# Optimization experiments

Measured on AMD Instinct MI355X. Metric: run time of the kernel, lower is better.

The kernel has to match this reference:

```python
import jax, jax.numpy as jnp
import numpy as np
from jax import lax

B, CIN, COUT, WDIM, K, H, W_ = 8, 512, 512, 512, 3, 64, 64

def setup_inputs() -> dict:
    key = jax.random.key(0)
    ks = jax.random.split(key, 7)
    x = jax.random.normal(ks[0], (B, CIN, H, W_), dtype=jnp.float32)
    w = jax.random.normal(ks[1], (B, WDIM), dtype=jnp.float32)
    noise = jax.random.normal(ks[2], (B, COUT, H, W_), dtype=jnp.float32)
    # params (kaiming-ish scale for weight; demodulation normalizes anyway)
    weight = jax.random.normal(ks[3], (1, COUT, CIN, K, K), dtype=jnp.float32) * 0.05
    affine_w = jax.random.normal(ks[4], (CIN, WDIM), dtype=jnp.float32) * (1.0 / np.sqrt(WDIM))
    affine_b = jnp.zeros((CIN,), dtype=jnp.float32)
    bias = jnp.zeros((COUT,), dtype=jnp.float32)
    return {"x": x, "w": w, "noise": noise, "weight": weight,
            "affine_w": affine_w, "affine_b": affine_b, "bias": bias}

def reference(x, w, noise, weight, affine_w, affine_b, bias):
    b, cin, h, ww = x.shape
    cout, k = weight.shape[1], weight.shape[3]
    # style: affine(w) + 1
    s = jnp.einsum('bd,cd->bc', w, affine_w) + affine_b          # [B, Cin]
    s = s[:, None, :, None, None] + 1.0                           # [B,1,Cin,1,1]
    w_mod = weight * s                                            # [B,Cout,Cin,k,k]
    d = lax.rsqrt(jnp.sum(w_mod * w_mod, axis=(2, 3, 4), keepdims=True) + 1e-8)
    w_mod = w_mod * d
    # grouped conv: groups = B
    x_ = x.reshape(1, b * cin, h, ww)
    w_ = w_mod.reshape(b * cout, cin, k, k)
    pad = k // 2
    y = lax.conv_general_dilated(
        x_, w_, window_strides=(1, 1), padding=[(pad, pad), (pad, pad)],
        feature_group_count=b,
        dimension_numbers=('NCHW', 'OIHW', 'NCHW'))
    y = y.reshape(b, cout, h, ww)
    y = y + noise + bias[None, :, None, None]
    return jnp.where(y >= 0, y, 0.2 * y)
```

## Files before the change

### kernel.cpp

```cpp
#include <hip/hip_runtime.h>
#include <hip/hip_bf16.h>


#define CIN   512
#define COUT  512
#define KDIM  4608
#define HWPIX 4096

typedef __attribute__((ext_vector_type(8))) __bf16 bf16x8;
typedef __attribute__((ext_vector_type(4))) float  f32x4;

__device__ __forceinline__ unsigned short f2bf(float f){
  union { float f; unsigned int u; } v; v.f = f;
  unsigned int u = v.u;
  u += 0x7fffu + ((u >> 16) & 1u);
  return (unsigned short)(u >> 16);
}

#define GLDS16(g, l) __builtin_amdgcn_global_load_lds(                      \
    (const __attribute__((address_space(1))) unsigned int*)(g),             \
    (__attribute__((address_space(3))) unsigned int*)(l), 16, 0, 0)

__global__ void style_k(const float* __restrict__ w, const float* __restrict__ aw,
                        const float* __restrict__ ab, float* __restrict__ styles){
  int wid = threadIdx.x >> 6, lane = threadIdx.x & 63;
  int gid = blockIdx.x * 4 + wid;
  int b = gid >> 9, c = gid & 511;
  const float* wb = w + b * 512;
  const float* ar = aw + c * 512;
  float sum = 0.f;
  for (int j = lane; j < 512; j += 64) sum += wb[j] * ar[j];
  for (int off = 32; off; off >>= 1) sum += __shfl_down(sum, off, 64);
  if (lane == 0) styles[gid] = sum + ab[c] + 1.0f;
}

__global__ void modw_k(const float* __restrict__ weight, const float* __restrict__ styles,
                       unsigned short* __restrict__ wmod){
  int o = blockIdx.x;
  int b = blockIdx.y;
  int t = threadIdx.x;
  const float* wrow = weight + (size_t)o * KDIM;
  const float* st = styles + b * 512;
  __shared__ unsigned short sw[9 * 520];
  __shared__ float red[4];
  int wid = t >> 6, lane = t & 63;
  float vals[18];
  float part = 0.f;
#pragma unroll
  for (int it = 0; it < 9; ++it){
    int e = (it * 256 + t) * 2;
    float2 v2 = *(const float2*)(wrow + e);
    int i0 = e / 9, i1 = (e + 1) / 9;
    float a0 = v2.x * st[i0];
    float a1 = v2.y * st[i1];
    vals[2 * it] = a0; vals[2 * it + 1] = a1;
    part += a0 * a0 + a1 * a1;
  }
  for (int off = 32; off; off >>= 1) part += __shfl_down(part, off, 64);
  if (lane == 0) red[wid] = part;
  __syncthreads();
  float d = rsqrtf(red[0] + red[1] + red[2] + red[3] + 1e-8f);
#pragma unroll
  for (int it = 0; it < 9; ++it){
    int e = (it * 256 + t) * 2;
    int i0 = e / 9, i1 = (e + 1) / 9;
    int tap0 = e - i0 * 9, tap1 = e + 1 - i1 * 9;
    sw[tap0 * 520 + i0] = f2bf(vals[2 * it] * d);
    sw[tap1 * 520 + i1] = f2bf(vals[2 * it + 1] * d);
  }
  __syncthreads();
  unsigned int* orow32 = (unsigned int*)(wmod + ((size_t)(b * 512 + o)) * KDIM);
#pragma unroll
  for (int it = 0; it < 9; ++it){
    int u = it * 256 + t;
    int e = u * 2;
    int tap2 = e >> 9, i2 = e & 511;
    orow32[u] = *(const unsigned int*)&sw[tap2 * 520 + i2];
  }
}

__global__ void xpose_k(const float* __restrict__ x, unsigned short* __restrict__ xpad){
  int h = blockIdx.x, cg = blockIdx.y, b = blockIdx.z;
  int c0 = cg * 64;
  __shared__ unsigned short lds[64][66];
  int t = threadIdx.x;
  const float* xb = x + (((size_t)(b * 512 + c0)) * 64 + h) * 64;
#pragma unroll
  for (int it = 0; it < 4; ++it){
    int idx = it * 256 + t;
    int cl = idx >> 4, w4 = (idx & 15) * 4;
    float4 v = *(const float4*)(xb + (size_t)cl * 4096 + w4);
    lds[w4 + 0][cl] = f2bf(v.x);
    lds[w4 + 1][cl] = f2bf(v.y);
    lds[w4 + 2][cl] = f2bf(v.z);
    lds[w4 + 3][cl] = f2bf(v.w);
  }
  if (t < 64){
    int which = t >> 5;
    int ch2 = (t & 31) * 2;
    int wl = which ? 65 : 0;
    *(unsigned int*)&xpad[(((size_t)b * 66 + h + 1) * 66 + wl) * 512 + c0 + ch2] = 0u;
  }
  if (h == 0 || h == 63){
    int row = (h == 0) ? 0 : 65;
    for (int u = t; u < 66 * 32; u += 256){
      int wl = u >> 5, ch2 = (u & 31) * 2;
      *(unsigned int*)&xpad[(((size_t)b * 66 + row) * 66 + wl) * 512 + c0 + ch2] = 0u;
    }
  }
  __syncthreads();
#pragma unroll
  for (int it = 0; it < 2; ++it){
    int idx = it * 256 + t;
    int wl = idx >> 3, ch = idx & 7;
    unsigned int u0 = *(const unsigned int*)&lds[wl][ch * 8 + 0];
    unsigned int u1 = *(const unsigned int*)&lds[wl][ch * 8 + 2];
    unsigned int u2 = *(const unsigned int*)&lds[wl][ch * 8 + 4];
    unsigned int u3 = *(const unsigned int*)&lds[wl][ch * 8 + 6];
    int off = ((b * 66 + h + 1) * 66 + (wl + 1)) * 512 + c0 + ch * 8;
    *(uint4*)&xpad[off] = make_uint4(u0, u1, u2, u3);
  }
}

__device__ __forceinline__ int bshift_of(int t){
  int tap = t >> 3;
  int dy = (tap * 11) >> 5;
  int dx = tap - dy * 3;
  return (((dy - 1) * 66 + (dx - 1)) << 9) + ((t & 7) << 6);
}

__global__ __launch_bounds__(512, 2) void conv_gemm(
    const unsigned short* __restrict__ wmod, const unsigned short* __restrict__ xpad,
    const float* __restrict__ noise, const float* __restrict__ bias,
    float* __restrict__ out){
  __shared__ unsigned short As[4][128 * 64];
  __shared__ unsigned short Bs[4][128 * 64];
  int g = blockIdx.x;
  int b = g & 7, sl = g >> 3;
  int mt = sl >> 4, nt = sl & 15;
  int m0 = mt * 256, n0 = nt * 256, h0 = nt * 4;
  int tid = threadIdx.x, lane = tid & 63, wid = tid >> 6;
  int wmp = wid >> 2, wnp = wid & 3;
  int lf = lane & 15, lg = lane >> 4;

  const unsigned short* wbase = wmod + ((size_t)(b * 512 + m0)) * KDIM;
  const unsigned short* xb    = xpad + (size_t)b * (66 * 66 * 512);

  int srow  = tid >> 3;
  int sc    = (tid & 7) ^ (srow & 7);
  int aoffg  = srow * KDIM + sc * 8;
  int boffg0 = ((h0 + 1) * 66 + srow + 1) * 512 + sc * 8;
  int boffg1 = ((h0 + 2) * 66 + srow + 1) * 512 + sc * 8;

  int arow[4], brow[2];
#pragma unroll
  for (int i = 0; i < 4; ++i) arow[i] = (wmp * 64 + i * 16 + lf) * 64;
#pragma unroll
  for (int j = 0; j < 2; ++j) brow[j] = (wnp * 32 + j * 16 + lf) * 64;
  int pch0 = ((lg    ) ^ (lane & 7)) * 8;
  int pch1 = ((lg + 4) ^ (lane & 7)) * 8;

  f32x4 acc[2][2][4][2];
#pragma unroll
  for (int a0 = 0; a0 < 2; ++a0)
#pragma unroll
    for (int a1 = 0; a1 < 2; ++a1)
#pragma unroll
      for (int a2 = 0; a2 < 4; ++a2)
#pragma unroll
        for (int a3 = 0; a3 < 2; ++a3) acc[a0][a1][a2][a3] = (f32x4){0.f, 0.f, 0.f, 0.f};

  bf16x8 af[4][2], bq0[2][2], bq1[2][2];

#define SBAR0() __builtin_amdgcn_sched_barrier(0)

#define STAGE_A(t_, h_, s_) do {                                              \
    const unsigned short* gpa_ = wbase + (size_t)(h_) * (128 * KDIM) + (t_) * 64; \
    GLDS16(gpa_ + aoffg,             &As[s_][tid * 8]);                       \
    GLDS16(gpa_ + aoffg + 64 * KDIM, &As[s_][(512 + tid) * 8]);               \
  } while (0)

#define STAGE_B(t_, h_, s_) do {                                              \
    const unsigned short* gpb_ = xb + (h_) * (2 * 66 * 512) + bshift_of(t_);  \
    GLDS16(gpb_ + boffg0, &Bs[s_][tid * 8]);                                  \
    GLDS16(gpb_ + boffg1, &Bs[s_][(512 + tid) * 8]);                          \
  } while (0)

#define LOAD_A(s_) do {                                                       \
    _Pragma("unroll") for (int fi_ = 0; fi_ < 4; ++fi_){                      \
      af[fi_][0] = *(const bf16x8*)&As[s_][arow[fi_] + pch0];                 \
      af[fi_][1] = *(const bf16x8*)&As[s_][arow[fi_] + pch1]; }               \
  } while (0)

#define LOAD_B(s_, B_) do {                                                   \
    _Pragma("unroll") for (int fj_ = 0; fj_ < 2; ++fj_){                      \
      B_[fj_][0] = *(const bf16x8*)&Bs[s_][brow[fj_] + pch0];                 \
      B_[fj_][1] = *(const bf16x8*)&Bs[s_][brow[fj_] + pch1]; }               \
  } while (0)

#define MFMA_Q(MH_, NH_, B_) do {                                             \
    __builtin_amdgcn_s_setprio(1);                                            \
    _Pragma("unroll") for (int fi_ = 0; fi_ < 4; ++fi_)                       \
    _Pragma("unroll") for (int fj_ = 0; fj_ < 2; ++fj_){                      \
      acc[MH_][NH_][fi_][fj_] = __builtin_amdgcn_mfma_f32_16x16x32_bf16(      \
          af[fi_][0], B_[fj_][0], acc[MH_][NH_][fi_][fj_], 0, 0, 0);          \
      acc[MH_][NH_][fi_][fj_] = __builtin_amdgcn_mfma_f32_16x16x32_bf16(      \
          af[fi_][1], B_[fj_][1], acc[MH_][NH_][fi_][fj_], 0, 0, 0); }        \
    __builtin_amdgcn_s_setprio(0);                                            \
  } while (0)

#define SYNC_MID() do { SBAR0(); __builtin_amdgcn_s_barrier();                \
    asm volatile("s_waitcnt lgkmcnt(0)" ::: "memory"); SBAR0(); } while (0)
#define SYNC_END() do { SBAR0(); __builtin_amdgcn_s_barrier(); } while (0)
#define VMW6() asm volatile("s_waitcnt vmcnt(6)" ::: "memory")
#define VMW0() asm volatile("s_waitcnt vmcnt(0)" ::: "memory")

  STAGE_A(0, 0, 0); STAGE_B(0, 0, 0); STAGE_B(0, 1, 1); STAGE_A(0, 1, 1);
  STAGE_A(1, 0, 2); STAGE_B(1, 0, 2); STAGE_B(1, 1, 3);
  VMW6();
  __builtin_amdgcn_s_barrier();

#pragma unroll 1
  for (int it = 0; it < 35; ++it){
    int T = it * 2;
    LOAD_A(0); LOAD_B(0, bq0);
    STAGE_A(T + 1, 1, 3);
    SYNC_MID(); MFMA_Q(0, 0, bq0); SYNC_END();
    LOAD_B(1, bq1);
    STAGE_A(T + 2, 0, 0);
    SYNC_MID(); MFMA_Q(0, 1, bq1); SYNC_END();
    LOAD_A(1);
    STAGE_B(T + 2, 0, 0);
    SYNC_MID(); MFMA_Q(1, 0, bq0); SYNC_END();
    STAGE_B(T + 2, 1, 1);
    VMW6();
    SYNC_MID(); MFMA_Q(1, 1, bq1); SYNC_END();
    LOAD_A(2); LOAD_B(2, bq0);
    STAGE_A(T + 2, 1, 1);
    SYNC_MID(); MFMA_Q(0, 0, bq0); SYNC_END();
    LOAD_B(3, bq1);
    STAGE_A(T + 3, 0, 2);
    SYNC_MID(); MFMA_Q(0, 1, bq1); SYNC_END();
    LOAD_A(3);
    STAGE_B(T + 3, 0, 2);
    SYNC_MID(); MFMA_Q(1, 0, bq0); SYNC_END();
    STAGE_B(T + 3, 1, 3);
    VMW6();
    SYNC_MID(); MFMA_Q(1, 1, bq1); SYNC_END();
  }

  LOAD_A(0); LOAD_B(0, bq0);
  STAGE_A(71, 1, 3);
  SYNC_MID(); MFMA_Q(0, 0, bq0); SYNC_END();
  LOAD_B(1, bq1);
  SYNC_MID(); MFMA_Q(0, 1, bq1); SYNC_END();
  LOAD_A(1);
  SYNC_MID(); MFMA_Q(1, 0, bq0); SYNC_END();
  VMW0();
  SYNC_MID(); MFMA_Q(1, 1, bq1); SYNC_END();
  LOAD_A(2); LOAD_B(2, bq0);
  SYNC_MID(); MFMA_Q(0, 0, bq0); SYNC_END();
  LOAD_B(3, bq1);
  SYNC_MID(); MFMA_Q(0, 1, bq1); SYNC_END();
  LOAD_A(3);
  SYNC_MID(); MFMA_Q(1, 0, bq0); SYNC_END();
  SYNC_MID(); MFMA_Q(1, 1, bq1);

#undef STAGE_A
#undef STAGE_B
#undef LOAD_A
#undef LOAD_B
#undef MFMA_Q
#undef SYNC_MID
#undef SYNC_END
#undef VMW6
#undef VMW0
#undef SBAR0

#pragma unroll
  for (int MH = 0; MH < 2; ++MH)
#pragma unroll
    for (int NH = 0; NH < 2; ++NH)
#pragma unroll
      for (int fi = 0; fi < 4; ++fi)
#pragma unroll
        for (int fj = 0; fj < 2; ++fj){
          int o_base = m0 + MH * 128 + wmp * 64 + fi * 16 + lg * 4;
          int n = n0 + NH * 128 + wnp * 32 + fj * 16 + lf;
#pragma unroll
          for (int r = 0; r < 4; ++r){
            int o = o_base + r;
            size_t idx = ((size_t)(b * 512 + o)) * HWPIX + n;
            float v = acc[MH][NH][fi][fj][r] + noise[idx] + bias[o];
            out[idx] = (v >= 0.f) ? v : 0.2f * v;
          }
        }
}

extern "C" void kernel_launch(void* const* d_in, const int* in_sizes, int n_in,
                              void* d_out, int out_size, void* d_ws, size_t ws_size,
                              hipStream_t stream) {
  const float* x        = (const float*)d_in[0];
  const float* w        = (const float*)d_in[1];
  const float* noise    = (const float*)d_in[2];
  const float* weight   = (const float*)d_in[3];
  const float* affine_w = (const float*)d_in[4];
  const float* affine_b = (const float*)d_in[5];
  const float* bias     = (const float*)d_in[6];
  float* out = (float*)d_out;

  float* styles = (float*)d_ws;
  unsigned short* wmod = (unsigned short*)((char*)d_ws + 16384);
  unsigned short* xpad = (unsigned short*)((char*)d_ws + 16384 + 37748736ull);

  style_k<<<dim3(1024), 256, 0, stream>>>(w, affine_w, affine_b, styles);
  modw_k <<<dim3(512, 8), 256, 0, stream>>>(weight, styles, wmod);
  xpose_k<<<dim3(64, 8, 8), 256, 0, stream>>>(x, xpad);
  conv_gemm<<<dim3(256), 512, 0, stream>>>(wmod, xpad, noise, bias, out);
}
```

Before: 326.5 us.

## Double-buffer A fragments and overlap LDS reads with MFMA phases

Adds a second register buffer for A fragments so the LDS reads for the next phase are issued before the current MFMA block. Partial lgkmcnt waits replace full waits, and one of the two barriers per phase is dropped. The global-to-LDS staging order and vmcnt thresholds are rearranged to match. This aims to hide LDS latency and barrier stalls behind matrix work, at the cost of more VGPRs and tighter reliance on getting the wait counts right.

```diff
diff --git a/kernel.cpp b/kernel.cpp
--- a/kernel.cpp
+++ b/kernel.cpp
@@ -170,7 +170,7 @@
 #pragma unroll
         for (int a3 = 0; a3 < 2; ++a3) acc[a0][a1][a2][a3] = (f32x4){0.f, 0.f, 0.f, 0.f};
 
-  bf16x8 af[4][2], bq0[2][2], bq1[2][2];
+  bf16x8 af0[4][2], af1[4][2], bq0[2][2], bq1[2][2];
 
 #define SBAR0() __builtin_amdgcn_sched_barrier(0)
 
@@ -186,94 +186,97 @@
     GLDS16(gpb_ + boffg1, &Bs[s_][(512 + tid) * 8]);                          \
   } while (0)
 
-#define LOAD_A(s_) do {                                                       \
-    _Pragma("unroll") for (int fi_ = 0; fi_ < 4; ++fi_){                      \
-      af[fi_][0] = *(const bf16x8*)&As[s_][arow[fi_] + pch0];                 \
-      af[fi_][1] = *(const bf16x8*)&As[s_][arow[fi_] + pch1]; }               \
-  } while (0)
-
-#define LOAD_B(s_, B_) do {                                                   \
+#define LOAD_AF1(AF_, s_, fi_) do {                                           \
+    AF_[fi_][0] = *(const bf16x8*)&As[s_][arow[fi_] + pch0];                  \
+    AF_[fi_][1] = *(const bf16x8*)&As[s_][arow[fi_] + pch1];                  \
+  } while (0)
+
+#define LOAD_BQ(B_, s_) do {                                                  \
     _Pragma("unroll") for (int fj_ = 0; fj_ < 2; ++fj_){                      \
       B_[fj_][0] = *(const bf16x8*)&Bs[s_][brow[fj_] + pch0];                 \
       B_[fj_][1] = *(const bf16x8*)&Bs[s_][brow[fj_] + pch1]; }               \
   } while (0)
 
-#define MFMA_Q(MH_, NH_, B_) do {                                             \
+#define MFMA_Q(MH_, NH_, AF_, B_) do {                                        \
     __builtin_amdgcn_s_setprio(1);                                            \
     _Pragma("unroll") for (int fi_ = 0; fi_ < 4; ++fi_)                       \
     _Pragma("unroll") for (int fj_ = 0; fj_ < 2; ++fj_){                      \
       acc[MH_][NH_][fi_][fj_] = __builtin_amdgcn_mfma_f32_16x16x32_bf16(      \
-          af[fi_][0], B_[fj_][0], acc[MH_][NH_][fi_][fj_], 0, 0, 0);          \
+          AF_[fi_][0], B_[fj_][0], acc[MH_][NH_][fi_][fj_], 0, 0, 0);         \
       acc[MH_][NH_][fi_][fj_] = __builtin_amdgcn_mfma_f32_16x16x32_bf16(      \
-          af[fi_][1], B_[fj_][1], acc[MH_][NH_][fi_][fj_], 0, 0, 0); }        \
+          AF_[fi_][1], B_[fj_][1], acc[MH_][NH_][fi_][fj_], 0, 0, 0); }       \
     __builtin_amdgcn_s_setprio(0);                                            \
   } while (0)
 
-#define SYNC_MID() do { SBAR0(); __builtin_amdgcn_s_barrier();                \
+#define TAIL6() do { SBAR0();                                                 \
+    asm volatile("s_waitcnt lgkmcnt(6)" ::: "memory"); SBAR0(); } while (0)
+#define TAIL0() do { SBAR0();                                                 \
     asm volatile("s_waitcnt lgkmcnt(0)" ::: "memory"); SBAR0(); } while (0)
-#define SYNC_END() do { SBAR0(); __builtin_amdgcn_s_barrier(); } while (0)
-#define VMW6() asm volatile("s_waitcnt vmcnt(6)" ::: "memory")
+#define PH_END() do { SBAR0(); __builtin_amdgcn_s_barrier(); } while (0)
+#define VMW4() asm volatile("s_waitcnt vmcnt(4)" ::: "memory")
 #define VMW0() asm volatile("s_waitcnt vmcnt(0)" ::: "memory")
 
-  STAGE_A(0, 0, 0); STAGE_B(0, 0, 0); STAGE_B(0, 1, 1); STAGE_A(0, 1, 1);
-  STAGE_A(1, 0, 2); STAGE_B(1, 0, 2); STAGE_B(1, 1, 3);
-  VMW6();
+  STAGE_A(0, 0, 0); STAGE_A(0, 1, 1); STAGE_B(0, 0, 0); STAGE_B(0, 1, 1);
+  STAGE_A(1, 0, 2); STAGE_B(1, 0, 2); STAGE_B(1, 1, 3); STAGE_A(1, 1, 3);
+  VMW0();
   __builtin_amdgcn_s_barrier();
+  LOAD_AF1(af0, 0, 0); LOAD_AF1(af0, 0, 1); LOAD_AF1(af0, 0, 2); LOAD_AF1(af0, 0, 3);
+  LOAD_BQ(bq0, 0);
 
 #pragma unroll 1
   for (int it = 0; it < 35; ++it){
     int T = it * 2;
-    LOAD_A(0); LOAD_B(0, bq0);
-    STAGE_A(T + 1, 1, 3);
-    SYNC_MID(); MFMA_Q(0, 0, bq0); SYNC_END();
-    LOAD_B(1, bq1);
-    STAGE_A(T + 2, 0, 0);
-    SYNC_MID(); MFMA_Q(0, 1, bq1); SYNC_END();
-    LOAD_A(1);
-    STAGE_B(T + 2, 0, 0);
-    SYNC_MID(); MFMA_Q(1, 0, bq0); SYNC_END();
+    LOAD_BQ(bq1, 1); LOAD_AF1(af1, 1, 0);
+    TAIL6(); MFMA_Q(0, 0, af0, bq0); PH_END();
+    STAGE_A(T + 2, 0, 0); STAGE_B(T + 2, 0, 0);
+    LOAD_AF1(af1, 1, 1); LOAD_AF1(af1, 1, 2); LOAD_AF1(af1, 1, 3);
+    TAIL6(); MFMA_Q(0, 1, af0, bq1); PH_END();
     STAGE_B(T + 2, 1, 1);
-    VMW6();
-    SYNC_MID(); MFMA_Q(1, 1, bq1); SYNC_END();
-    LOAD_A(2); LOAD_B(2, bq0);
+    LOAD_AF1(af0, 2, 0); LOAD_AF1(af0, 2, 1); LOAD_AF1(af0, 2, 2);
+    TAIL6(); MFMA_Q(1, 0, af1, bq0); PH_END();
     STAGE_A(T + 2, 1, 1);
-    SYNC_MID(); MFMA_Q(0, 0, bq0); SYNC_END();
-    LOAD_B(3, bq1);
-    STAGE_A(T + 3, 0, 2);
-    SYNC_MID(); MFMA_Q(0, 1, bq1); SYNC_END();
-    LOAD_A(3);
-    STAGE_B(T + 3, 0, 2);
-    SYNC_MID(); MFMA_Q(1, 0, bq0); SYNC_END();
+    VMW4();
+    LOAD_BQ(bq0, 2); LOAD_AF1(af0, 2, 3);
+    TAIL6(); MFMA_Q(1, 1, af1, bq1); PH_END();
+    LOAD_BQ(bq1, 3); LOAD_AF1(af1, 3, 0);
+    TAIL6(); MFMA_Q(0, 0, af0, bq0); PH_END();
+    STAGE_A(T + 3, 0, 2); STAGE_B(T + 3, 0, 2);
+    LOAD_AF1(af1, 3, 1); LOAD_AF1(af1, 3, 2); LOAD_AF1(af1, 3, 3);
+    TAIL6(); MFMA_Q(0, 1, af0, bq1); PH_END();
     STAGE_B(T + 3, 1, 3);
-    VMW6();
-    SYNC_MID(); MFMA_Q(1, 1, bq1); SYNC_END();
-  }
-
-  LOAD_A(0); LOAD_B(0, bq0);
-  STAGE_A(71, 1, 3);
-  SYNC_MID(); MFMA_Q(0, 0, bq0); SYNC_END();
-  LOAD_B(1, bq1);
-  SYNC_MID(); MFMA_Q(0, 1, bq1); SYNC_END();
-  LOAD_A(1);
-  SYNC_MID(); MFMA_Q(1, 0, bq0); SYNC_END();
+    LOAD_AF1(af0, 0, 0); LOAD_AF1(af0, 0, 1); LOAD_AF1(af0, 0, 2);
+    TAIL6(); MFMA_Q(1, 0, af1, bq0); PH_END();
+    STAGE_A(T + 3, 1, 3);
+    VMW4();
+    LOAD_BQ(bq0, 0); LOAD_AF1(af0, 0, 3);
+    TAIL6(); MFMA_Q(1, 1, af1, bq1); PH_END();
+  }
+
+  LOAD_BQ(bq1, 1); LOAD_AF1(af1, 1, 0);
+  TAIL6(); MFMA_Q(0, 0, af0, bq0); PH_END();
+  LOAD_AF1(af1, 1, 1); LOAD_AF1(af1, 1, 2); LOAD_AF1(af1, 1, 3);
+  TAIL6(); MFMA_Q(0, 1, af0, bq1); PH_END();
+  LOAD_AF1(af0, 2, 0); LOAD_AF1(af0, 2, 1); LOAD_AF1(af0, 2, 2);
+  TAIL6(); MFMA_Q(1, 0, af1, bq0); PH_END();
   VMW0();
-  SYNC_MID(); MFMA_Q(1, 1, bq1); SYNC_END();
-  LOAD_A(2); LOAD_B(2, bq0);
-  SYNC_MID(); MFMA_Q(0, 0, bq0); SYNC_END();
-  LOAD_B(3, bq1);
-  SYNC_MID(); MFMA_Q(0, 1, bq1); SYNC_END();
-  LOAD_A(3);
-  SYNC_MID(); MFMA_Q(1, 0, bq0); SYNC_END();
-  SYNC_MID(); MFMA_Q(1, 1, bq1);
+  LOAD_BQ(bq0, 2); LOAD_AF1(af0, 2, 3);
+  TAIL6(); MFMA_Q(1, 1, af1, bq1); PH_END();
+  LOAD_BQ(bq1, 3); LOAD_AF1(af1, 3, 0);
+  TAIL6(); MFMA_Q(0, 0, af0, bq0); PH_END();
+  LOAD_AF1(af1, 3, 1); LOAD_AF1(af1, 3, 2); LOAD_AF1(af1, 3, 3);
+  TAIL6(); MFMA_Q(0, 1, af0, bq1); PH_END();
+  TAIL0(); MFMA_Q(1, 0, af1, bq0); PH_END();
+  TAIL0(); MFMA_Q(1, 1, af1, bq1);
 
 #undef STAGE_A
 #undef STAGE_B
-#undef LOAD_A
-#undef LOAD_B
+#undef LOAD_AF1
+#undef LOAD_BQ
 #undef MFMA_Q
-#undef SYNC_MID
-#undef SYNC_END
-#undef VMW6
+#undef TAIL6
+#undef TAIL0
+#undef PH_END
+#undef VMW4
 #undef VMW0
 #undef SBAR0
 
```

New measurement: 338.0 us. 1.04x slower.
